# Kernel tuning notes

Measured on AMD Instinct MI355X. Metric: run time of the kernel, lower is better.

## Reference

```python
import jax, jax.numpy as jnp
import numpy as np

BN_EPS = 1e-5
LEAKY_SLOPE = 0.1


def conv_bn_leaky(x, w, gamma, beta, mean, var, pad):
    # Conv2d(no bias) + BatchNorm2d(inference) + LeakyReLU(0.1), NCHW/OIHW
    y = jax.lax.conv_general_dilated(
        x, w, window_strides=(1, 1), padding=[(pad, pad), (pad, pad)],
        dimension_numbers=("NCHW", "OIHW", "NCHW"))
    scale = gamma / jnp.sqrt(var + BN_EPS)
    shift = beta - mean * scale
    y = y * scale[None, :, None, None] + shift[None, :, None, None]
    return jnp.where(y > 0, y, LEAKY_SLOPE * y)


def reorg(x, s=2):
    # vedanet Reorg: out[b, (a*s+d)*C + c, i, j] = x[b, c, i*s+a, j*s+d]
    B, C, H, W = x.shape
    Ho, Wo = H // s, W // s
    return x.reshape(B, C, Ho, s, Wo, s).transpose(0, 3, 5, 1, 2, 4).reshape(B, s * s * C, Ho, Wo)


def setup_inputs() -> dict:
    key = jax.random.key(0)
    ks = jax.random.split(key, 10)
    B, H, W = 32, 19, 19
    NC, NA = 20, 5
    return {
        "stage6": jax.random.normal(ks[0], (B, 1024, H, W), jnp.float32),
        "stage5": jax.random.normal(ks[1], (B, 512, 2 * H, 2 * W), jnp.float32),
        "w1": jax.random.normal(ks[2], (64, 512, 1, 1), jnp.float32) * 0.05,
        "g1": jnp.ones((64,), jnp.float32),
        "b1": jnp.zeros((64,), jnp.float32),
        "m1": jax.random.normal(ks[3], (64,), jnp.float32) * 0.1,
        "v1": jax.random.uniform(ks[4], (64,), jnp.float32, 0.5, 1.5),
        "w2": jax.random.normal(ks[5], (1024, 1280, 3, 3), jnp.float32) * 0.02,
        "g2": jnp.ones((1024,), jnp.float32),
        "b2": jnp.zeros((1024,), jnp.float32),
        "m2": jax.random.normal(ks[6], (1024,), jnp.float32) * 0.1,
        "v2": jax.random.uniform(ks[7], (1024,), jnp.float32, 0.5, 1.5),
        "meta_state": jax.random.normal(ks[8], (NC, NA * 6, 1025), jnp.float32) * 0.05,
    }


def reference(stage6, stage5, w1, g1, b1, m1, v1, w2, g2, b2, m2, v2, meta_state):
    # layers[0]: 1x1 conv-bn-leaky on stage5, then Reorg(2) -> (B, 256, H, W)
    x = conv_bn_leaky(stage5, w1, g1, b1, m1, v1, pad=0)
    x = reorg(x, 2)
    # layers[1]: 3x3 conv-bn-leaky on concat -> (B, 1024, H, W)
    pre = conv_bn_leaky(jnp.concatenate([x, stage6], axis=1), w2, g2, b2, m2, v2, pad=1)
    # meta_predict: per-class 1x1 conv, batched as one einsum
    cls_w = meta_state[:, :, :-1]   # (NC, NA*6, 1024)
    cls_b = meta_state[:, :, -1]    # (NC, NA*6)
    out = jnp.einsum("bkij,cmk->bcmij", pre, cls_w) + cls_b[None, :, :, None, None]
    B, NC, M = pre.shape[0], meta_state.shape[0], meta_state.shape[1]
    return out.reshape(B * NC, M, pre.shape[2], pre.shape[3])
```

## Files before the change

kernel.cpp:

```cpp
#include <hip/hip_runtime.h>

typedef unsigned short u16;
typedef unsigned int   u32;

typedef __attribute__((ext_vector_type(8))) short bf16x8;
typedef __attribute__((ext_vector_type(4))) float f32x4;

__device__ __forceinline__ u16 f2bf(float f) {
  u32 u = __float_as_uint(f);
  u32 r = (u + 0x7fffu + ((u >> 16) & 1u)) >> 16;
  return (u16)r;
}

__device__ __forceinline__ void async16(const void* g, void* l) {
  __builtin_amdgcn_global_load_lds(
      (const __attribute__((address_space(1))) u32*)g,
      (__attribute__((address_space(3))) u32*)l, 16, 0, 0);
}

__global__ __launch_bounds__(256) void mega_prep_kern(
    const float* __restrict__ stage5, const float* __restrict__ s6,
    const float* __restrict__ w1,
    const float* __restrict__ g1, const float* __restrict__ b1,
    const float* __restrict__ m1, const float* __restrict__ v1,
    const float* __restrict__ w2, const float* __restrict__ g2,
    const float* __restrict__ b2, const float* __restrict__ m2,
    const float* __restrict__ v2, const float* __restrict__ meta,
    u16* __restrict__ in_bf, u16* __restrict__ w2p,
    u16* __restrict__ clsp, float* __restrict__ clsb,
    float* __restrict__ shift2)
{
  __shared__ __align__(16) char smem[8704];
  const int bid = blockIdx.x;
  const int t = threadIdx.x;

  if (bid < 722) {
    float* sc_s = (float*)smem;
    float* sh_s = (float*)(smem + 256);
    char*  aT   = smem + 512;
    char*  bT   = smem + 4608;
    const int w = t >> 6, lane = t & 63;
    if (t < 64) {
      float s = g1[t] * rsqrtf(v1[t] + 1e-5f);
      sc_s[t] = s;
      sh_s[t] = b1[t] - m1[t] * s;
    }
    const int m0 = bid * 64;
    const int pS = t & 63, gS = t >> 6;
    const int mS = m0 + pS;
    const int bS = mS / 1444, hwS = mS - bS * 1444;
    const float* s5 = stage5 + (size_t)bS * (512 * 1444) + hwS;
    const int ocA = t >> 2, icqA = t & 3;
    const float* w1r = w1 + (size_t)ocA * 512 + icqA * 8;
    char* aW = aT + (ocA >> 4) * 1024 + (icqA * 16 + (ocA & 15)) * 16;
    char* bW = bT + pS * 64 + ((gS ^ ((pS >> 1) & 3))) * 16;
    const int bR = (w * 16 + (lane & 15)) * 64 +
                   (((lane >> 4) ^ (((lane & 15) >> 1) & 3))) * 16;
    f32x4 acc[4] = {};
    __syncthreads();
    const float sA = sc_s[ocA];
    for (int kc = 0; kc < 16; ++kc) {
      const int ic0 = kc * 32;
      float a8[8], b8[8];
#pragma unroll
      for (int e = 0; e < 8; ++e) a8[e] = w1r[ic0 + e];
#pragma unroll
      for (int e = 0; e < 8; ++e) b8[e] = s5[(size_t)(ic0 + gS * 8 + e) * 1444];
      __syncthreads();
      uint4 av, bv;
      av.x = (u32)f2bf(a8[0] * sA) | ((u32)f2bf(a8[1] * sA) << 16);
      av.y = (u32)f2bf(a8[2] * sA) | ((u32)f2bf(a8[3] * sA) << 16);
      av.z = (u32)f2bf(a8[4] * sA) | ((u32)f2bf(a8[5] * sA) << 16);
      av.w = (u32)f2bf(a8[6] * sA) | ((u32)f2bf(a8[7] * sA) << 16);
      bv.x = (u32)f2bf(b8[0]) | ((u32)f2bf(b8[1]) << 16);
      bv.y = (u32)f2bf(b8[2]) | ((u32)f2bf(b8[3]) << 16);
      bv.z = (u32)f2bf(b8[4]) | ((u32)f2bf(b8[5]) << 16);
      bv.w = (u32)f2bf(b8[6]) | ((u32)f2bf(b8[7]) << 16);
      *(uint4*)aW = av;
      *(uint4*)bW = bv;
      __syncthreads();
      bf16x8 bfv = *(const bf16x8*)(bT + bR);
#pragma unroll
      for (int i = 0; i < 4; ++i) {
        bf16x8 af = *(const bf16x8*)(aT + i * 1024 + lane * 16);
        acc[i] = __builtin_amdgcn_mfma_f32_16x16x32_bf16(af, bfv, acc[i], 0, 0, 0);
      }
    }
    const int mE = m0 + w * 16 + (lane & 15);
    const int bE = mE / 1444, hwE = mE - bE * 1444;
    const int h = hwE / 38, wq = hwE - h * 38;
    const int ho = h >> 1, wo = wq >> 1, q = ((h & 1) << 1) | (wq & 1);
    u16* dst = in_bf + (((size_t)bE * 21 + 1 + ho) * 21 + 1 + wo) * 1280 + q * 64;
    const int lq = lane >> 4;
#pragma unroll
    for (int i = 0; i < 4; ++i) {
      int oc = i * 16 + lq * 4;
      float v0 = acc[i][0] + sh_s[oc + 0]; v0 = v0 > 0.f ? v0 : 0.1f * v0;
      float v1_ = acc[i][1] + sh_s[oc + 1]; v1_ = v1_ > 0.f ? v1_ : 0.1f * v1_;
      float v2_ = acc[i][2] + sh_s[oc + 2]; v2_ = v2_ > 0.f ? v2_ : 0.1f * v2_;
      float v3 = acc[i][3] + sh_s[oc + 3]; v3 = v3 > 0.f ? v3 : 0.1f * v3;
      u32 lo = (u32)f2bf(v0) | ((u32)f2bf(v1_) << 16);
      u32 hi = (u32)f2bf(v2_) | ((u32)f2bf(v3) << 16);
      u32* dp = (u32*)(dst + oc);
      dp[0] = lo; dp[1] = hi;
    }
    return;
  }

  if (bid < 3794) {
    u16 (*tile)[66] = (u16(*)[66])smem;
    const int sub = bid - 722;
    const int jt = sub % 6, ct = (sub / 6) % 16, b = sub / 96;
    const int ij0 = jt * 64, c0 = ct * 64;
    const int col = t & 63, rr = t >> 6;
#pragma unroll
    for (int r = 0; r < 16; ++r) {
      int cl = r * 4 + rr;
      int ij = ij0 + col;
      float v = 0.f;
      if (ij < 361) v = s6[((size_t)b * 1024 + c0 + cl) * 361 + ij];
      tile[cl][col] = f2bf(v);
    }
    __syncthreads();
#pragma unroll
    for (int r = 0; r < 16; ++r) {
      int ijl = r * 4 + rr;
      int ij = ij0 + ijl;
      if (ij < 361) {
        int i = ij / 19, j = ij - i * 19;
        in_bf[(((size_t)b * 21 + 1 + i) * 21 + 1 + j) * 1280 + 256 + c0 + col] =
            tile[col][ijl];
      }
    }
    return;
  }

  if (bid < 5394) {
    int gi = (bid - 3794) * 256 + t;
    int b = gi / 12800;
    int rem = gi - b * 12800;
    int p = rem / 160, qq = rem - p * 160;
    int row, col;
    if (p < 21)      { row = 0;      col = p; }
    else if (p < 42) { row = 20;     col = p - 21; }
    else if (p < 61) { row = p - 41; col = 0; }
    else             { row = p - 60; col = 20; }
    uint4 z = {0u, 0u, 0u, 0u};
    *(uint4*)(in_bf + (((size_t)b * 21 + row) * 21 + col) * 1280 + qq * 8) = z;
    return;
  }

  if (bid < 7794) {
    int idx = (bid - 5394) * 256 + t;
    int cm = idx >> 10, k = idx & 1023;
    int tile_ = cm >> 7, g = (cm >> 4) & 7, mm = cm & 15;
    int kc = k >> 5, ksub = (k >> 3) & 3, e = k & 7;
    size_t dst = (((size_t)tile_ * 32 + kc) * 8 + g) * 512
                 + (size_t)(ksub * 16 + mm) * 8 + e;
    clsp[dst] = f2bf(meta[(size_t)cm * 1025 + k]);
    if (idx < 600) clsb[idx] = meta[(size_t)idx * 1025 + 1024];
    if (idx < 1024) {
      float sc = g2[idx] * rsqrtf(v2[idx] + 1e-5f);
      shift2[idx] = b2[idx] - m2[idx] * sc;
    }
    return;
  }

  {
    u16* tile = (u16*)smem;
    const int sub = bid - 7794;
    const int icb = sub % 10;
    const int oc = sub / 10;
    const int ic0 = icb * 128;
    const float sc = g2[oc] * rsqrtf(v2[oc] + 1e-5f);
    const float* src = w2 + (size_t)oc * 11520 + (size_t)ic0 * 9;
#pragma unroll
    for (int p = t; p < 1152; p += 256) {
      float v = src[p];
      int ic_l = p / 9;
      int khw = p - ic_l * 9;
      tile[khw * 130 + ic_l] = f2bf(v * sc);
    }
    __syncthreads();
    if (t < 144) {
      int khw = t >> 4, c = (t >> 2) & 3, ksub = t & 3;
      int kt = khw * 40 + icb * 4 + c;
      const u16* s = &tile[khw * 130 + c * 32 + ksub * 8];
      uint4 v;
      v.x = (u32)s[0] | ((u32)s[1] << 16);
      v.y = (u32)s[2] | ((u32)s[3] << 16);
      v.z = (u32)s[4] | ((u32)s[5] << 16);
      v.w = (u32)s[6] | ((u32)s[7] << 16);
      int oc_l = oc & 255;
      size_t dst = (((size_t)(oc >> 8) * 360 + kt) * 2 + (oc_l >> 7)) * 4096
                   + (size_t)(((oc_l >> 4) & 7) * 64 + ksub * 16 + (oc & 15)) * 8;
      *(uint4*)(w2p + dst) = v;
    }
  }
}

__global__ __launch_bounds__(512, 2) void conv2_gemm_kern(
    const u16* __restrict__ Wp, const u16* __restrict__ Ig,
    const float* __restrict__ shift2, u16* __restrict__ pre)
{
  __shared__ u16 As[4][8192];
  __shared__ u16 Bs[4][8192];
  __shared__ float shft[256];

  const int t = threadIdx.x;
  const int w = t >> 6, lane = t & 63;
  const int wm = w >> 2, wn = w & 3;

  const int s = ((blockIdx.x & 7) * 23) + (blockIdx.x >> 3);
  const int mTile = s >> 2, ocTile = s & 3;
  const int m0 = mTile * 256, oc0 = ocTile * 256;

  const int rw = t >> 2;
  const int rpart = ((t & 3) ^ ((t >> 3) & 3)) * 8;
  int mA = m0 + rw;        if (mA > 11551) mA = 11551;
  int mB = m0 + 128 + rw;  if (mB > 11551) mB = 11551;
  const int bA = mA / 361, ijA = mA - bA * 361;
  const int ohA = ijA / 19, owA = ijA - ohA * 19;
  const int bB = mB / 361, ijB = mB - bB * 361;
  const int ohB = ijB / 19, owB = ijB - ohB * 19;
  const u16* pI0 = Ig + (size_t)((bA * 21 + ohA) * 21 + owA) * 1280 + rpart;
  const u16* pI1 = Ig + (size_t)((bB * 21 + ohB) * 21 + owB) * 1280 + rpart;

  const u16* pW = Wp + (size_t)ocTile * 2949120 + (size_t)t * 8;

  const int aOff = wm * 4096 + lane * 8;
  const int bOff = (wn * 64 + (lane & 15)) * 32 +
                   (((lane >> 4) ^ ((lane >> 1) & 3)) * 8);

  int skh = 0, skw = 0, sicb = 0, sIo = 0;

#pragma unroll
  for (int st = 0; st < 3; ++st) {
    async16(pW + (size_t)st * 8192,        &As[st][t * 8]);
    async16(pI0 + sIo,                     &Bs[st][t * 8]);
    async16(pW + (size_t)st * 8192 + 4096, &As[st][4096 + t * 8]);
    async16(pI1 + sIo,                     &Bs[st][4096 + t * 8]);
    ++sicb; sIo += 32;
    if (sicb == 40) { sicb = 0; ++skw; if (skw == 3) { skw = 0; ++skh; }
                      sIo = (skh * 21 + skw) * 1280; }
  }
  asm volatile("s_waitcnt vmcnt(8)" ::: "memory");
  __builtin_amdgcn_s_barrier();

  f32x4 acc[8][4] = {};

  for (int kt = 0; kt < 360; ++kt) {
    const int cb = kt & 3;
    const u16* Ab = As[cb];
    const u16* Bb = Bs[cb];
    const int stb = (kt + 3) & 3;
    const int st = (kt > 356) ? 359 : kt + 3;
    const size_t aSrc = (size_t)st * 8192;

    bf16x8 af[4], bfv[4];
#pragma unroll
    for (int i = 0; i < 4; ++i)
      af[i] = *(const bf16x8*)&Ab[aOff + i * 512];
#pragma unroll
    for (int j = 0; j < 4; ++j)
      bfv[j] = *(const bf16x8*)&Bb[bOff + j * 512];
    async16(pW + aSrc, &As[stb][t * 8]);
    async16(pI0 + sIo, &Bs[stb][t * 8]);
    __builtin_amdgcn_s_barrier();
    asm volatile("s_waitcnt lgkmcnt(0)" ::: "memory");
    __builtin_amdgcn_sched_barrier(0);
    __builtin_amdgcn_s_setprio(1);
#pragma unroll
    for (int i = 0; i < 4; ++i)
#pragma unroll
      for (int j = 0; j < 4; ++j)
        acc[i][j] = __builtin_amdgcn_mfma_f32_16x16x32_bf16(
            af[i], bfv[j], acc[i][j], 0, 0, 0);
    __builtin_amdgcn_s_setprio(0);
    __builtin_amdgcn_s_barrier();

#pragma unroll
    for (int i = 0; i < 4; ++i)
      af[i] = *(const bf16x8*)&Ab[aOff + 2048 + i * 512];
    async16(pW + aSrc + 4096, &As[stb][4096 + t * 8]);
    async16(pI1 + sIo,        &Bs[stb][4096 + t * 8]);
    __builtin_amdgcn_s_barrier();
    asm volatile("s_waitcnt lgkmcnt(0)" ::: "memory");
    __builtin_amdgcn_sched_barrier(0);
    __builtin_amdgcn_s_setprio(1);
#pragma unroll
    for (int i = 0; i < 4; ++i)
#pragma unroll
      for (int j = 0; j < 4; ++j)
        acc[4 + i][j] = __builtin_amdgcn_mfma_f32_16x16x32_bf16(
            af[i], bfv[j], acc[4 + i][j], 0, 0, 0);
    __builtin_amdgcn_s_setprio(0);
    asm volatile("s_waitcnt vmcnt(8)" ::: "memory");
    __builtin_amdgcn_s_barrier();

    ++sicb; sIo += 32;
    if (sicb == 40) { sicb = 0; ++skw; if (skw == 3) { skw = 0; ++skh; }
                      sIo = (skh * 21 + skw) * 1280; }
  }

  if (t < 256) shft[t] = shift2[oc0 + t];
  __syncthreads();

  const int lq = lane >> 4, lr = lane & 15;
#pragma unroll
  for (int j = 0; j < 4; ++j) {
    const int m = m0 + wn * 64 + j * 16 + lr;
    if (m >= 11552) continue;
    u16* prow = pre + (size_t)m * 1024 + oc0 + wm * 128;
#pragma unroll
    for (int i = 0; i < 8; ++i) {
      const int ocl = i * 16 + lq * 4;
      float v0 = acc[i][j][0] + shft[wm * 128 + ocl + 0]; v0 = v0 > 0.f ? v0 : 0.1f * v0;
      float v1 = acc[i][j][1] + shft[wm * 128 + ocl + 1]; v1 = v1 > 0.f ? v1 : 0.1f * v1;
      float v2 = acc[i][j][2] + shft[wm * 128 + ocl + 2]; v2 = v2 > 0.f ? v2 : 0.1f * v2;
      float v3 = acc[i][j][3] + shft[wm * 128 + ocl + 3]; v3 = v3 > 0.f ? v3 : 0.1f * v3;
      u32 lo = (u32)f2bf(v0) | ((u32)f2bf(v1) << 16);
      u32 hi = (u32)f2bf(v2) | ((u32)f2bf(v3) << 16);
      u32* dp = (u32*)(prow + ocl);
      dp[0] = lo; dp[1] = hi;
    }
  }
}

__global__ __launch_bounds__(256) void einsum_gemm_kern(
    const u16* __restrict__ Ap, const u16* __restrict__ Bg,
    const float* __restrict__ biasg, float* __restrict__ out)
{
  __shared__ u16 Wa[128 * 32];
  __shared__ u16 Ib[128 * 32];
  __shared__ float sbias[128];
  const int t = threadIdx.x;
  const int w = t >> 6, lane = t & 63;
  const int m0 = blockIdx.x * 128;
  const int cm0 = blockIdx.y * 128;
  if (t < 128) { int c = cm0 + t; sbias[t] = (c < 600) ? biasg[c] : 0.f; }

  const u16* pA0 = Ap + ((size_t)(cm0 >> 7) * 256 + w) * 512 + lane * 8;

  const int rw = t >> 2;
  const int rpart = ((t & 3) ^ ((t >> 3) & 3)) * 8;
  int rB0 = m0 + rw;        if (rB0 > 11551) rB0 = 11551;
  int rB1 = m0 + 64 + rw;   if (rB1 > 11551) rB1 = 11551;
  const u16* pB0 = Bg + (size_t)rB0 * 1024 + rpart;
  const u16* pB1 = Bg + (size_t)rB1 * 1024 + rpart;

  u16* waS0 = &Wa[w * 512];
  u16* waS1 = &Wa[2048 + w * 512];
  u16* ibS0 = &Ib[w * 512];
  u16* ibS1 = &Ib[2048 + w * 512];

  const int aBase = (w >> 1) * 2048 + lane * 8;
  const int bBase = (w & 1) * 2048 + (lane & 15) * 32 +
                    (((lane >> 4) ^ ((lane >> 1) & 3))) * 8;

  f32x4 acc[4][4] = {};

  for (int kt = 0; kt < 32; ++kt) {
    const size_t off = (size_t)kt * 32;
    async16(pA0 + (size_t)kt * 4096, waS0);
    async16(pA0 + (size_t)kt * 4096 + 2048, waS1);
    async16(pB0 + off, ibS0);
    async16(pB1 + off, ibS1);
    __syncthreads();
    bf16x8 af[4], bfv[4];
#pragma unroll
    for (int i = 0; i < 4; ++i)
      af[i] = *(const bf16x8*)&Wa[aBase + i * 512];
#pragma unroll
    for (int j = 0; j < 4; ++j)
      bfv[j] = *(const bf16x8*)&Ib[bBase + j * 512];
#pragma unroll
    for (int i = 0; i < 4; ++i)
#pragma unroll
      for (int j = 0; j < 4; ++j)
        acc[i][j] = __builtin_amdgcn_mfma_f32_16x16x32_bf16(
            af[i], bfv[j], acc[i][j], 0, 0, 0);
    __syncthreads();
  }

  const int aRow = (w >> 1) * 64, bRow = (w & 1) * 64;
  const int lq = lane >> 4, lr = lane & 15;
#pragma unroll
  for (int j = 0; j < 4; ++j) {
    int m = m0 + bRow + j * 16 + lr;
    if (m >= 11552) continue;
    int b = m / 361, ij = m - b * 361;
    float* obase = out + (size_t)b * 216600 + ij;
#pragma unroll
    for (int i = 0; i < 4; ++i) {
      int cml = aRow + i * 16 + lq * 4;
#pragma unroll
      for (int r = 0; r < 4; ++r) {
        int cm = cm0 + cml + r;
        if (cm < 600) obase[(size_t)cm * 361] = acc[i][j][r] + sbias[cml + r];
      }
    }
  }
}

extern "C" void kernel_launch(void* const* d_in, const int* in_sizes, int n_in,
                              void* d_out, int out_size, void* d_ws, size_t ws_size,
                              hipStream_t stream)
{
  const float* stage6 = (const float*)d_in[0];
  const float* stage5 = (const float*)d_in[1];
  const float* w1 = (const float*)d_in[2];
  const float* g1 = (const float*)d_in[3];
  const float* b1 = (const float*)d_in[4];
  const float* m1 = (const float*)d_in[5];
  const float* v1 = (const float*)d_in[6];
  const float* w2 = (const float*)d_in[7];
  const float* g2 = (const float*)d_in[8];
  const float* b2 = (const float*)d_in[9];
  const float* m2 = (const float*)d_in[10];
  const float* v2 = (const float*)d_in[11];
  const float* meta = (const float*)d_in[12];
  float* out = (float*)d_out;

  char* ws = (char*)d_ws;
  u16*   in_bf  = (u16*)(ws);
  u16*   w2p    = (u16*)(ws + 36126720);
  u16*   prebf  = (u16*)(ws + 59719680);
  u16*   clsp   = (u16*)(ws + 83378176);
  float* clsb   = (float*)(ws + 84688896);
  float* shift2 = (float*)(ws + 84691456);

  mega_prep_kern<<<18034, 256, 0, stream>>>(
      stage5, stage6, w1, g1, b1, m1, v1, w2, g2, b2, m2, v2, meta,
      in_bf, w2p, clsp, clsb, shift2);
  conv2_gemm_kern<<<184, 512, 0, stream>>>(w2p, in_bf, shift2, prebf);
  einsum_gemm_kern<<<dim3(91, 5), 256, 0, stream>>>(clsp, prebf, clsb, out);
}
```

Baseline: 591.8 us.

## Register-double-buffer conv2 GEMM fragments and cut barriers per K-tile

Restructures the conv2 implicit-GEMM main loop so the next K-tile's A and B fragments are read from LDS while the current tile's MFMAs run. Two B register buffers alternate via a macro unrolled twice. The per-tile barriers and lgkmcnt waits drop from four to one combined vmcnt+barrier. The goal is to hide LDS read latency behind MFMAs and remove synchronization stalls, at the cost of more registers under the 2-blocks-per-CU launch bound and a subtler buffer-reuse ordering that could introduce races.

```diff
diff --git a/kernel.cpp b/kernel.cpp
--- a/kernel.cpp
+++ b/kernel.cpp
@@ -199,6 +199,56 @@
   }
 }
 
+#define CONV2_TILE(BCUR, BNXT)                                              \
+  {                                                                         \
+    const int cb = kt & 3, nb = (kt + 1) & 3, stb = stile & 3;              \
+    const size_t aSrc = (size_t)stile * 8192;                               \
+         \
+    async16(pW + aSrc, &As[stb][t * 8]);                                    \
+    async16(pI0 + sIo, &Bs[stb][t * 8]);                                    \
+    _Pragma("unroll")                                                       \
+    for (int i = 0; i < 4; ++i)                                             \
+      afB[i] = *(const bf16x8*)&As[cb][aOff + 2048 + i * 512];              \
+    __builtin_amdgcn_sched_barrier(0);                                      \
+    __builtin_amdgcn_s_setprio(1);                                          \
+    _Pragma("unroll")                                                       \
+    for (int i = 0; i < 4; ++i)                                             \
+      _Pragma("unroll")                                                     \
+      for (int j = 0; j < 4; ++j)                                           \
+        acc[i][j] = __builtin_amdgcn_mfma_f32_16x16x32_bf16(                \
+            afA[i], BCUR[j], acc[i][j], 0, 0, 0);                           \
+    __builtin_amdgcn_s_setprio(0);                                          \
+          \
+    async16(pW + aSrc + 4096, &As[stb][4096 + t * 8]);                      \
+    async16(pI1 + sIo, &Bs[stb][4096 + t * 8]);                             \
+    _Pragma("unroll")                                                       \
+    for (int i = 0; i < 4; ++i)                                             \
+      afA[i] = *(const bf16x8*)&As[nb][aOff + i * 512];                     \
+    _Pragma("unroll")                                                       \
+    for (int j = 0; j < 4; ++j)                                             \
+      BNXT[j] = *(const bf16x8*)&Bs[nb][bOff + j * 512];                    \
+    __builtin_amdgcn_sched_barrier(0);                                      \
+    __builtin_amdgcn_s_setprio(1);                                          \
+    _Pragma("unroll")                                                       \
+    for (int i = 0; i < 4; ++i)                                             \
+      _Pragma("unroll")                                                     \
+      for (int j = 0; j < 4; ++j)                                           \
+        acc[4 + i][j] = __builtin_amdgcn_mfma_f32_16x16x32_bf16(            \
+            afB[i], BCUR[j], acc[4 + i][j], 0, 0, 0);                       \
+    __builtin_amdgcn_s_setprio(0);                                          \
+       \
+    asm volatile("s_waitcnt vmcnt(4)\n\ts_barrier" ::: "memory");           \
+    if (stile < 359) {                                                      \
+      ++stile; ++sicb; sIo += 32;                                           \
+      if (sicb == 40) {                                                     \
+        sicb = 0; ++skw;                                                    \
+        if (skw == 3) { skw = 0; ++skh; }                                   \
+        sIo = (skh * 21 + skw) * 1280;                                      \
+      }                                                                     \
+    }                                                                       \
+    ++kt;                                                                   \
+  }
+
 __global__ __launch_bounds__(512, 2) void conv2_gemm_kern(
     const u16* __restrict__ Wp, const u16* __restrict__ Ig,
     const float* __restrict__ shift2, u16* __restrict__ pre)
@@ -232,75 +282,32 @@
   const int bOff = (wn * 64 + (lane & 15)) * 32 +
                    (((lane >> 4) ^ ((lane >> 1) & 3)) * 8);
 
-  int skh = 0, skw = 0, sicb = 0, sIo = 0;
-
-#pragma unroll
-  for (int st = 0; st < 3; ++st) {
-    async16(pW + (size_t)st * 8192,        &As[st][t * 8]);
-    async16(pI0 + sIo,                     &Bs[st][t * 8]);
-    async16(pW + (size_t)st * 8192 + 4096, &As[st][4096 + t * 8]);
-    async16(pI1 + sIo,                     &Bs[st][4096 + t * 8]);
-    ++sicb; sIo += 32;
-    if (sicb == 40) { sicb = 0; ++skw; if (skw == 3) { skw = 0; ++skh; }
-                      sIo = (skh * 21 + skw) * 1280; }
-  }
-  asm volatile("s_waitcnt vmcnt(8)" ::: "memory");
-  __builtin_amdgcn_s_barrier();
+  int stile = 0, sicb = 0, skh = 0, skw = 0, sIo = 0;
+
+#pragma unroll
+  for (int p = 0; p < 3; ++p) {
+    async16(pW + (size_t)stile * 8192,        &As[p][t * 8]);
+    async16(pI0 + sIo,                        &Bs[p][t * 8]);
+    async16(pW + (size_t)stile * 8192 + 4096, &As[p][4096 + t * 8]);
+    async16(pI1 + sIo,                        &Bs[p][4096 + t * 8]);
+    ++stile; ++sicb; sIo += 32;
+  }
+  asm volatile("s_waitcnt vmcnt(4)\n\ts_barrier" ::: "memory");
+
+  bf16x8 afA[4], afB[4], b0[4], b1[4];
+#pragma unroll
+  for (int i = 0; i < 4; ++i)
+    afA[i] = *(const bf16x8*)&As[0][aOff + i * 512];
+#pragma unroll
+  for (int j = 0; j < 4; ++j)
+    b0[j] = *(const bf16x8*)&Bs[0][bOff + j * 512];
 
   f32x4 acc[8][4] = {};
 
-  for (int kt = 0; kt < 360; ++kt) {
-    const int cb = kt & 3;
-    const u16* Ab = As[cb];
-    const u16* Bb = Bs[cb];
-    const int stb = (kt + 3) & 3;
-    const int st = (kt > 356) ? 359 : kt + 3;
-    const size_t aSrc = (size_t)st * 8192;
-
-    bf16x8 af[4], bfv[4];
-#pragma unroll
-    for (int i = 0; i < 4; ++i)
-      af[i] = *(const bf16x8*)&Ab[aOff + i * 512];
-#pragma unroll
-    for (int j = 0; j < 4; ++j)
-      bfv[j] = *(const bf16x8*)&Bb[bOff + j * 512];
-    async16(pW + aSrc, &As[stb][t * 8]);
-    async16(pI0 + sIo, &Bs[stb][t * 8]);
-    __builtin_amdgcn_s_barrier();
-    asm volatile("s_waitcnt lgkmcnt(0)" ::: "memory");
-    __builtin_amdgcn_sched_barrier(0);
-    __builtin_amdgcn_s_setprio(1);
-#pragma unroll
-    for (int i = 0; i < 4; ++i)
-#pragma unroll
-      for (int j = 0; j < 4; ++j)
-        acc[i][j] = __builtin_amdgcn_mfma_f32_16x16x32_bf16(
-            af[i], bfv[j], acc[i][j], 0, 0, 0);
-    __builtin_amdgcn_s_setprio(0);
-    __builtin_amdgcn_s_barrier();
-
-#pragma unroll
-    for (int i = 0; i < 4; ++i)
-      af[i] = *(const bf16x8*)&Ab[aOff + 2048 + i * 512];
-    async16(pW + aSrc + 4096, &As[stb][4096 + t * 8]);
-    async16(pI1 + sIo,        &Bs[stb][4096 + t * 8]);
-    __builtin_amdgcn_s_barrier();
-    asm volatile("s_waitcnt lgkmcnt(0)" ::: "memory");
-    __builtin_amdgcn_sched_barrier(0);
-    __builtin_amdgcn_s_setprio(1);
-#pragma unroll
-    for (int i = 0; i < 4; ++i)
-#pragma unroll
-      for (int j = 0; j < 4; ++j)
-        acc[4 + i][j] = __builtin_amdgcn_mfma_f32_16x16x32_bf16(
-            af[i], bfv[j], acc[4 + i][j], 0, 0, 0);
-    __builtin_amdgcn_s_setprio(0);
-    asm volatile("s_waitcnt vmcnt(8)" ::: "memory");
-    __builtin_amdgcn_s_barrier();
-
-    ++sicb; sIo += 32;
-    if (sicb == 40) { sicb = 0; ++skw; if (skw == 3) { skw = 0; ++skh; }
-                      sIo = (skh * 21 + skw) * 1280; }
+  int kt = 0;
+  for (int k2 = 0; k2 < 180; ++k2) {
+    CONV2_TILE(b0, b1)
+    CONV2_TILE(b1, b0)
   }
 
   if (t < 256) shft[t] = shift2[oc0 + t];
```

After: 627.2 us. +6.0%, slower.

## Retile conv2 GEMM to 384x128 tiles with double-buffered 64-wide K steps

Applied to the files above, without the earlier changes.

Changes the conv2 implicit-GEMM tile from 256x256 (M x OC) to 384x128, launching 248 blocks instead of 184 so the work spreads more evenly across the CUs. Each warp now owns a 48-row M strip. The pipeline drops from a 4-stage ring of 32-wide K slices to a 2-stage double buffer of 64-wide K slices, halving the loop trip count to 180. Launch bounds drop to one block per SM because the LDS footprint grows, which trades occupancy for better balance and fewer barriers per unit of K.

```diff
diff --git a/kernel.cpp b/kernel.cpp
--- a/kernel.cpp
+++ b/kernel.cpp
@@ -199,73 +199,72 @@
   }
 }
 
-__global__ __launch_bounds__(512, 2) void conv2_gemm_kern(
+__global__ __launch_bounds__(512, 1) void conv2_gemm_kern(
     const u16* __restrict__ Wp, const u16* __restrict__ Ig,
     const float* __restrict__ shift2, u16* __restrict__ pre)
 {
-  __shared__ u16 As[4][8192];
-  __shared__ u16 Bs[4][8192];
-  __shared__ float shft[256];
+  __shared__ u16 As[2][8192];
+  __shared__ u16 Bs[2][24576];
+  __shared__ float shft[128];
 
   const int t = threadIdx.x;
   const int w = t >> 6, lane = t & 63;
-  const int wm = w >> 2, wn = w & 3;
-
-  const int s = ((blockIdx.x & 7) * 23) + (blockIdx.x >> 3);
-  const int mTile = s >> 2, ocTile = s & 3;
-  const int m0 = mTile * 256, oc0 = ocTile * 256;
+
+  const int s = ((blockIdx.x & 7) * 31) + (blockIdx.x >> 3);
+  const int mTile = s >> 3, ocTile = s & 7;
+  const int m0 = mTile * 384, oc0 = ocTile * 128;
 
   const int rw = t >> 2;
   const int rpart = ((t & 3) ^ ((t >> 3) & 3)) * 8;
   int mA = m0 + rw;        if (mA > 11551) mA = 11551;
   int mB = m0 + 128 + rw;  if (mB > 11551) mB = 11551;
+  int mC = m0 + 256 + rw;  if (mC > 11551) mC = 11551;
   const int bA = mA / 361, ijA = mA - bA * 361;
   const int ohA = ijA / 19, owA = ijA - ohA * 19;
   const int bB = mB / 361, ijB = mB - bB * 361;
   const int ohB = ijB / 19, owB = ijB - ohB * 19;
+  const int bC = mC / 361, ijC = mC - bC * 361;
+  const int ohC = ijC / 19, owC = ijC - ohC * 19;
   const u16* pI0 = Ig + (size_t)((bA * 21 + ohA) * 21 + owA) * 1280 + rpart;
   const u16* pI1 = Ig + (size_t)((bB * 21 + ohB) * 21 + owB) * 1280 + rpart;
-
-  const u16* pW = Wp + (size_t)ocTile * 2949120 + (size_t)t * 8;
-
-  const int aOff = wm * 4096 + lane * 8;
-  const int bOff = (wn * 64 + (lane & 15)) * 32 +
+  const u16* pI2 = Ig + (size_t)((bC * 21 + ohC) * 21 + owC) * 1280 + rpart;
+
+  const u16* pW = Wp + (size_t)(ocTile >> 1) * (360 * 8192)
+                     + (size_t)(ocTile & 1) * 4096 + (size_t)t * 8;
+
+  const int aOff = lane * 8;
+  const int bOff = (w * 48 + (lane & 15)) * 32 +
                    (((lane >> 4) ^ ((lane >> 1) & 3)) * 8);
 
-  int skh = 0, skw = 0, sicb = 0, sIo = 0;
-
-#pragma unroll
-  for (int st = 0; st < 3; ++st) {
-    async16(pW + (size_t)st * 8192,        &As[st][t * 8]);
-    async16(pI0 + sIo,                     &Bs[st][t * 8]);
-    async16(pW + (size_t)st * 8192 + 4096, &As[st][4096 + t * 8]);
-    async16(pI1 + sIo,                     &Bs[st][4096 + t * 8]);
-    ++sicb; sIo += 32;
-    if (sicb == 40) { sicb = 0; ++skw; if (skw == 3) { skw = 0; ++skh; }
-                      sIo = (skh * 21 + skw) * 1280; }
-  }
-  asm volatile("s_waitcnt vmcnt(8)" ::: "memory");
-  __builtin_amdgcn_s_barrier();
-
-  f32x4 acc[8][4] = {};
-
-  for (int kt = 0; kt < 360; ++kt) {
-    const int cb = kt & 3;
-    const u16* Ab = As[cb];
-    const u16* Bb = Bs[cb];
-    const int stb = (kt + 3) & 3;
-    const int st = (kt > 356) ? 359 : kt + 3;
-    const size_t aSrc = (size_t)st * 8192;
-
-    bf16x8 af[4], bfv[4];
-#pragma unroll
-    for (int i = 0; i < 4; ++i)
-      af[i] = *(const bf16x8*)&Ab[aOff + i * 512];
-#pragma unroll
-    for (int j = 0; j < 4; ++j)
-      bfv[j] = *(const bf16x8*)&Bb[bOff + j * 512];
-    async16(pW + aSrc, &As[stb][t * 8]);
-    async16(pI0 + sIo, &Bs[stb][t * 8]);
+  async16(pW,                 &As[0][t * 8]);
+  async16(pI0,                &Bs[0][t * 8]);
+  async16(pI1,                &Bs[0][4096 + t * 8]);
+  async16(pI2,                &Bs[0][8192 + t * 8]);
+  async16(pW + 8192,          &As[0][4096 + t * 8]);
+  async16(pI0 + 32,           &Bs[0][12288 + t * 8]);
+  async16(pI1 + 32,           &Bs[0][12288 + 4096 + t * 8]);
+  async16(pI2 + 32,           &Bs[0][12288 + 8192 + t * 8]);
+  asm volatile("s_waitcnt vmcnt(4)\n\ts_barrier" ::: "memory");
+
+  f32x4 acc[8][3] = {};
+
+  for (int kt = 0; kt < 180; ++kt) {
+    const int cb = kt & 1, nb = cb ^ 1;
+    const int stile = (kt < 179) ? kt + 1 : 179;
+    const int khwN = stile / 20, pairN = stile - khwN * 20;
+    const int khN = khwN / 3, kwN = khwN - khN * 3;
+    const size_t sIoN = (size_t)((khN * 21 + kwN) * 1280) + (size_t)pairN * 64;
+    const size_t aN = (size_t)stile * 16384;
+
+    bf16x8 aflo[4], afhi[4], bf[3];
+
+#pragma unroll
+    for (int i = 0; i < 4; ++i)
+      aflo[i] = *(const bf16x8*)&As[cb][aOff + i * 512];
+#pragma unroll
+    for (int j = 0; j < 3; ++j)
+      bf[j] = *(const bf16x8*)&Bs[cb][bOff + j * 512];
+    async16(pW + aN, &As[nb][t * 8]);
     __builtin_amdgcn_s_barrier();
     asm volatile("s_waitcnt lgkmcnt(0)" ::: "memory");
     __builtin_amdgcn_sched_barrier(0);
@@ -273,17 +272,18 @@
 #pragma unroll
     for (int i = 0; i < 4; ++i)
 #pragma unroll
-      for (int j = 0; j < 4; ++j)
+      for (int j = 0; j < 3; ++j)
         acc[i][j] = __builtin_amdgcn_mfma_f32_16x16x32_bf16(
-            af[i], bfv[j], acc[i][j], 0, 0, 0);
+            aflo[i], bf[j], acc[i][j], 0, 0, 0);
     __builtin_amdgcn_s_setprio(0);
     __builtin_amdgcn_s_barrier();
 
 #pragma unroll
     for (int i = 0; i < 4; ++i)
-      af[i] = *(const bf16x8*)&Ab[aOff + 2048 + i * 512];
-    async16(pW + aSrc + 4096, &As[stb][4096 + t * 8]);
-    async16(pI1 + sIo,        &Bs[stb][4096 + t * 8]);
+      afhi[i] = *(const bf16x8*)&As[cb][aOff + 2048 + i * 512];
+    async16(pI0 + sIoN, &Bs[nb][t * 8]);
+    async16(pI1 + sIoN, &Bs[nb][4096 + t * 8]);
+    async16(pI2 + sIoN, &Bs[nb][8192 + t * 8]);
     __builtin_amdgcn_s_barrier();
     asm volatile("s_waitcnt lgkmcnt(0)" ::: "memory");
     __builtin_amdgcn_sched_barrier(0);
@@ -291,34 +291,70 @@
 #pragma unroll
     for (int i = 0; i < 4; ++i)
 #pragma unroll
-      for (int j = 0; j < 4; ++j)
+      for (int j = 0; j < 3; ++j)
         acc[4 + i][j] = __builtin_amdgcn_mfma_f32_16x16x32_bf16(
-            af[i], bfv[j], acc[4 + i][j], 0, 0, 0);
+            afhi[i], bf[j], acc[4 + i][j], 0, 0, 0);
     __builtin_amdgcn_s_setprio(0);
-    asm volatile("s_waitcnt vmcnt(8)" ::: "memory");
-    __builtin_amdgcn_s_barrier();
-
-    ++sicb; sIo += 32;
-    if (sicb == 40) { sicb = 0; ++skw; if (skw == 3) { skw = 0; ++skh; }
-                      sIo = (skh * 21 + skw) * 1280; }
-  }
-
-  if (t < 256) shft[t] = shift2[oc0 + t];
+    asm volatile("s_waitcnt vmcnt(4)" ::: "memory");
+    __builtin_amdgcn_s_barrier();
+
+#pragma unroll
+    for (int i = 0; i < 4; ++i)
+      aflo[i] = *(const bf16x8*)&As[cb][4096 + aOff + i * 512];
+#pragma unroll
+    for (int j = 0; j < 3; ++j)
+      bf[j] = *(const bf16x8*)&Bs[cb][12288 + bOff + j * 512];
+    async16(pW + aN + 8192, &As[nb][4096 + t * 8]);
+    __builtin_amdgcn_s_barrier();
+    asm volatile("s_waitcnt lgkmcnt(0)" ::: "memory");
+    __builtin_amdgcn_sched_barrier(0);
+    __builtin_amdgcn_s_setprio(1);
+#pragma unroll
+    for (int i = 0; i < 4; ++i)
+#pragma unroll
+      for (int j = 0; j < 3; ++j)
+        acc[i][j] = __builtin_amdgcn_mfma_f32_16x16x32_bf16(
+            aflo[i], bf[j], acc[i][j], 0, 0, 0);
+    __builtin_amdgcn_s_setprio(0);
+    __builtin_amdgcn_s_barrier();
+
+#pragma unroll
+    for (int i = 0; i < 4; ++i)
+      afhi[i] = *(const bf16x8*)&As[cb][4096 + 2048 + aOff + i * 512];
+    async16(pI0 + sIoN + 32, &Bs[nb][12288 + t * 8]);
+    async16(pI1 + sIoN + 32, &Bs[nb][12288 + 4096 + t * 8]);
+    async16(pI2 + sIoN + 32, &Bs[nb][12288 + 8192 + t * 8]);
+    __builtin_amdgcn_s_barrier();
+    asm volatile("s_waitcnt lgkmcnt(0)" ::: "memory");
+    __builtin_amdgcn_sched_barrier(0);
+    __builtin_amdgcn_s_setprio(1);
+#pragma unroll
+    for (int i = 0; i < 4; ++i)
+#pragma unroll
+      for (int j = 0; j < 3; ++j)
+        acc[4 + i][j] = __builtin_amdgcn_mfma_f32_16x16x32_bf16(
+            afhi[i], bf[j], acc[4 + i][j], 0, 0, 0);
+    __builtin_amdgcn_s_setprio(0);
+    asm volatile("s_waitcnt vmcnt(4)" ::: "memory");
+    __builtin_amdgcn_s_barrier();
+  }
+
+  if (t < 128) shft[t] = shift2[oc0 + t];
   __syncthreads();
 
   const int lq = lane >> 4, lr = lane & 15;
 #pragma unroll
-  for (int j = 0; j < 4; ++j) {
-    const int m = m0 + wn * 64 + j * 16 + lr;
+  for (int j = 0; j < 3; ++j) {
+    const int m = m0 + w * 48 + j * 16 + lr;
     if (m >= 11552) continue;
-    u16* prow = pre + (size_t)m * 1024 + oc0 + wm * 128;
+    u16* prow = pre + (size_t)m * 1024 + oc0;
 #pragma unroll
     for (int i = 0; i < 8; ++i) {
       const int ocl = i * 16 + lq * 4;
-      float v0 = acc[i][j][0] + shft[wm * 128 + ocl + 0]; v0 = v0 > 0.f ? v0 : 0.1f * v0;
-      float v1 = acc[i][j][1] + shft[wm * 128 + ocl + 1]; v1 = v1 > 0.f ? v1 : 0.1f * v1;
-      float v2 = acc[i][j][2] + shft[wm * 128 + ocl + 2]; v2 = v2 > 0.f ? v2 : 0.1f * v2;
-      float v3 = acc[i][j][3] + shft[wm * 128 + ocl + 3]; v3 = v3 > 0.f ? v3 : 0.1f * v3;
+      float v0 = acc[i][j][0] + shft[ocl + 0]; v0 = v0 > 0.f ? v0 : 0.1f * v0;
+      float v1 = acc[i][j][1] + shft[ocl + 1]; v1 = v1 > 0.f ? v1 : 0.1f * v1;
+      float v2 = acc[i][j][2] + shft[ocl + 2]; v2 = v2 > 0.f ? v2 : 0.1f * v2;
+      float v3 = acc[i][j][3] + shft[ocl + 3]; v3 = v3 > 0.f ? v3 : 0.1f * v3;
       u32 lo = (u32)f2bf(v0) | ((u32)f2bf(v1) << 16);
       u32 hi = (u32)f2bf(v2) | ((u32)f2bf(v3) << 16);
       u32* dp = (u32*)(prow + ocl);
@@ -433,6 +469,6 @@
   mega_prep_kern<<<18034, 256, 0, stream>>>(
       stage5, stage6, w1, g1, b1, m1, v1, w2, g2, b2, m2, v2, meta,
       in_bf, w2p, clsp, clsb, shift2);
-  conv2_gemm_kern<<<184, 512, 0, stream>>>(w2p, in_bf, shift2, prebf);
+  conv2_gemm_kern<<<248, 512, 0, stream>>>(w2p, in_bf, shift2, prebf);
   einsum_gemm_kern<<<dim3(91, 5), 256, 0, stream>>>(clsp, prebf, clsb, out);
 }
```

New measurement: 669.0 us. 13.0% more time.
